# Optimization experiments

Hardware: AMD Instinct MI355X
Metric: run time of the kernel (lower is better)

## Reference

```python
import jax, jax.numpy as jnp
import numpy as np

MAX_SPAN_WIDTH = 30
NUM_WORDS = 2048
NUM_CAND = 8192
HIDDEN = 768
FEAT = 20
FFNN = 1000
SPAN_DIM = HIDDEN * 3 + FEAT  # 2324
TOP_SPAN_NUM = int(NUM_WORDS * 0.4)  # 819


def setup_inputs() -> dict:
    key = jax.random.key(0)
    ks = jax.random.split(key, 16)
    mention_doc = jax.random.normal(ks[0], (NUM_WORDS, HIDDEN), jnp.float32)
    starts = jax.random.randint(ks[1], (NUM_CAND,), 0, NUM_WORDS - MAX_SPAN_WIDTH, jnp.int32)
    widths = jax.random.randint(ks[2], (NUM_CAND,), 1, MAX_SPAN_WIDTH + 1, jnp.int32)
    ends = jnp.minimum(starts + widths - 1, NUM_WORDS - 1).astype(jnp.int32)
    s = 0.02
    lin = lambda k, i, o: jax.random.normal(k, (i, o), jnp.float32) * s
    return dict(
        mention_doc=mention_doc,
        span_width_emb=jax.random.normal(ks[3], (MAX_SPAN_WIDTH, FEAT), jnp.float32) * s,
        head_w=jax.random.normal(ks[4], (HIDDEN,), jnp.float32) * s,
        head_b=jnp.zeros((), jnp.float32),
        m_w1=lin(ks[5], SPAN_DIM, FFNN), m_b1=jnp.zeros((FFNN,), jnp.float32),
        m_w2=lin(ks[6], FFNN, FFNN), m_b2=jnp.zeros((FFNN,), jnp.float32),
        m_w3=jax.random.normal(ks[7], (FFNN,), jnp.float32) * s, m_b3=jnp.zeros((), jnp.float32),
        width_prior_emb=jax.random.normal(ks[8], (MAX_SPAN_WIDTH, FEAT), jnp.float32) * s,
        w_w1=lin(ks[9], FEAT, FFNN), w_b1=jnp.zeros((FFNN,), jnp.float32),
        w_w2=lin(ks[10], FFNN, FFNN), w_b2=jnp.zeros((FFNN,), jnp.float32),
        w_w3=jax.random.normal(ks[11], (FFNN,), jnp.float32) * s, w_b3=jnp.zeros((), jnp.float32),
        candidate_starts=starts,
        candidate_ends=ends,
        top_span_num=TOP_SPAN_NUM,
    )


def get_span_emb(mention_doc, starts, ends, span_width_emb, head_w, head_b):
    # mention_doc: [N, H]; starts/ends: [C]
    num_words = mention_doc.shape[0]
    start_emb = mention_doc[starts]              # [C, H]
    end_emb = mention_doc[ends]                  # [C, H]
    width_ids = ends - starts                    # span width - 1, in [0, MAX_SPAN_WIDTH)
    width_emb = span_width_emb[width_ids]        # [C, F]
    offs = jnp.arange(MAX_SPAN_WIDTH, dtype=starts.dtype)
    idxes = jnp.minimum(starts[:, None] + offs[None, :], num_words - 1)  # [C, W]
    emb_spans = mention_doc[idxes]               # [C, W, H]  (dominant intermediate)
    head_scores = mention_doc @ head_w + head_b  # [N]
    hs = head_scores[idxes]                      # [C, W]
    mask = offs[None, :] <= width_ids[:, None]
    hs = jnp.where(mask, hs, -jnp.inf)
    attn = jax.nn.softmax(hs, axis=1)            # masked softmax over span positions
    attended = jnp.einsum('cw,cwh->ch', attn, emb_spans)
    return jnp.concatenate([start_emb, end_emb, width_emb, attended], axis=-1)  # [C, 3H+F]


def ffnn3(x, w1, b1, w2, b2, w3, b3):
    h = jax.nn.relu(x @ w1 + b1)
    h = jax.nn.relu(h @ w2 + b2)
    return h @ w3 + b3  # [..., ] scalar score per row (Squeezer)


def extract_top_spans(span_scores, starts, ends, top_span_num, num_words):
    # Greedy crossing-interval NMS, faithful to the original sequential algorithm.
    C = span_scores.shape[0]
    order = jnp.argsort(-span_scores)
    offs = jnp.arange(MAX_SPAN_WIDTH, dtype=jnp.int32)

    def body(i, state):
        max_end, min_start, sel, count = state
        idx = order[i]
        s = starts[idx]
        e = ends[idx]
        dup = max_end[s] == e
        j_raw = s + offs
        j = jnp.minimum(j_raw, num_words - 1)
        in_span = j_raw <= e
        # crossing: an already-selected span starting at j>s ends beyond e,
        # or one ending at j<e starts before s.
        c1 = in_span & (j_raw > s) & (max_end[j] > e)
        c2 = in_span & (j_raw < e) & (min_start[j] < s)
        crossed = jnp.any(c1 | c2)
        accept = (~dup) & (~crossed) & (count < top_span_num)
        sel = jnp.where(accept, sel.at[count].set(idx.astype(jnp.int32)), sel)
        max_end = jnp.where(accept, max_end.at[s].max(e), max_end)
        min_start = jnp.where(accept, min_start.at[e].min(s), min_start)
        count = count + accept.astype(jnp.int32)
        return (max_end, min_start, sel, count)

    max_end0 = jnp.full((num_words,), -1, jnp.int32)          # 'not set' sentinel
    min_start0 = jnp.full((num_words,), num_words, jnp.int32)  # 'not set' sentinel
    sel0 = jnp.zeros((top_span_num,), jnp.int32)
    _, _, sel, count = jax.lax.fori_loop(0, C, body, (max_end0, min_start0, sel0, jnp.int32(0)))

    # sort selected spans by (start, end); pad unfilled slots with the first sorted span
    valid = jnp.arange(top_span_num) < count
    keys = jnp.where(valid, starts[sel] * num_words + ends[sel], jnp.iinfo(jnp.int32).max)
    sorted_sel = sel[jnp.argsort(keys)]
    return jnp.where(valid, sorted_sel, sorted_sel[0])


def reference(mention_doc, span_width_emb, head_w, head_b,
              m_w1, m_b1, m_w2, m_b2, m_w3, m_b3,
              width_prior_emb, w_w1, w_b1, w_w2, w_b2, w_w3, w_b3,
              candidate_starts, candidate_ends, top_span_num):
    num_words = mention_doc.shape[0]
    span_emb = get_span_emb(mention_doc, candidate_starts, candidate_ends,
                            span_width_emb, head_w, head_b)            # [C, 2324]
    mention_scores = ffnn3(span_emb, m_w1, m_b1, m_w2, m_b2, m_w3, m_b3)  # [C]
    width_scores = ffnn3(width_prior_emb, w_w1, w_b1, w_w2, w_b2, w_w3, w_b3)  # [30]
    cand_mention_scores = mention_scores + width_scores[candidate_ends - candidate_starts]
    top_idx = extract_top_spans(cand_mention_scores, candidate_starts, candidate_ends,
                                top_span_num, num_words)               # [top]
    top_starts = candidate_starts[top_idx]
    top_ends = candidate_ends[top_idx]
    top_span_emb = span_emb[top_idx]
    top_scores = cand_mention_scores[top_idx]
    return (cand_mention_scores, top_idx, top_starts, top_ends, top_span_emb, top_scores)
```

## Files before the change

### kernel.cpp

```cpp
#include <hip/hip_runtime.h>
#include <cstdio>
#include <cmath>

#define NUM_WORDS 2048
#define NUM_CAND 8192
#define HIDDEN 768
#define FEAT 20
#define FFNN_DIM 1000
#define SPAN_DIM 2324
#define TOP_NUM 819
#define MSW 30
#define KP2 1024
#define NP 1024
#define PNP 3072

#define OUT_TOPIDX   (NUM_CAND)
#define OUT_TSTART   (NUM_CAND + TOP_NUM)
#define OUT_TEND     (NUM_CAND + 2*TOP_NUM)
#define OUT_TEMB     (NUM_CAND + 3*TOP_NUM)
#define OUT_TSCORE   (NUM_CAND + 3*TOP_NUM + TOP_NUM*SPAN_DIM)

typedef short short8 __attribute__((ext_vector_type(8)));
typedef float f32x4 __attribute__((ext_vector_type(4)));
typedef unsigned short u16x4 __attribute__((ext_vector_type(4)));

__device__ __forceinline__ unsigned short bf16_rne(float x) {
    unsigned int u = __float_as_uint(x);
    unsigned int r = u + 0x7FFFu + ((u >> 16) & 1u);
    return (unsigned short)(r >> 16);
}
__device__ __forceinline__ float bf16_to_f(unsigned short h) {
    return __uint_as_float(((unsigned int)h) << 16);
}
__device__ __forceinline__ void store_split3(unsigned short* p0, unsigned short* p1,
                                             unsigned short* p2, size_t off, float v) {
    unsigned short h0 = bf16_rne(v);
    float r1 = v - bf16_to_f(h0);
    unsigned short h1 = bf16_rne(r1);
    float r2 = r1 - bf16_to_f(h1);
    p0[off] = h0;
    p1[off] = h1;
    p2[off] = bf16_rne(r2);
}

__device__ __forceinline__ void gl_lds16(const unsigned short* g, unsigned short* l) {
    __builtin_amdgcn_global_load_lds(
        (const __attribute__((address_space(1))) unsigned short*)g,
        (__attribute__((address_space(3))) unsigned short*)l, 16, 0, 0);
}

__global__ void head_kernel(const float* __restrict__ doc, const float* __restrict__ hw,
                            const float* __restrict__ hb, float* __restrict__ out) {
    int wave = threadIdx.x >> 6, lane = threadIdx.x & 63;
    int row = blockIdx.x * 4 + wave;
    if (row >= NUM_WORDS) return;
    float acc = 0.f;
    for (int h = lane; h < HIDDEN; h += 64) acc += doc[row * HIDDEN + h] * hw[h];
    for (int off = 32; off > 0; off >>= 1) acc += __shfl_down(acc, off);
    if (lane == 0) out[row] = acc + hb[0];
}

__global__ void width_kernel(const float* __restrict__ x, const float* __restrict__ w1,
                             const float* __restrict__ b1, const float* __restrict__ w2,
                             const float* __restrict__ b2, const float* __restrict__ w3,
                             const float* __restrict__ b3, float* __restrict__ out) {
    __shared__ float xs[FEAT];
    __shared__ float h1s[FFNN_DIM];
    __shared__ float red[256];
    int r = blockIdx.x, t = threadIdx.x;
    if (t < FEAT) xs[t] = x[r * FEAT + t];
    __syncthreads();
    for (int j = t; j < FFNN_DIM; j += 256) {
        float acc = b1[j];
        for (int k = 0; k < FEAT; ++k) acc += xs[k] * w1[k * FFNN_DIM + j];
        h1s[j] = fmaxf(acc, 0.f);
    }
    __syncthreads();
    float partial = 0.f;
    for (int j = t; j < FFNN_DIM; j += 256) {
        float acc = b2[j];
        for (int k = 0; k < FFNN_DIM; ++k) acc += h1s[k] * w2[k * FFNN_DIM + j];
        partial += fmaxf(acc, 0.f) * w3[j];
    }
    red[t] = partial;
    __syncthreads();
    for (int s = 128; s > 0; s >>= 1) { if (t < s) red[t] += red[t + s]; __syncthreads(); }
    if (t == 0) out[r] = red[0] + b3[0];
}

__global__ void attn_kernel(const float* __restrict__ head_s, const int* __restrict__ starts,
                            const int* __restrict__ ends, float* __restrict__ attn_g) {
    int wave = threadIdx.x >> 6, w = threadIdx.x & 63;
    int c = blockIdx.x * 4 + wave;
    if (c >= NUM_CAND) return;
    int s = starts[c], e = ends[c];
    int wid = e - s;
    float hsv = -INFINITY;
    if (w < MSW && w <= wid) hsv = head_s[s + w];
    float m = hsv;
    for (int off = 32; off > 0; off >>= 1) m = fmaxf(m, __shfl_down(m, off));
    m = __shfl(m, 0);
    float ex = (w < MSW && w <= wid) ? expf(hsv - m) : 0.f;
    float ssum = ex;
    for (int off = 32; off > 0; off >>= 1) ssum += __shfl_down(ssum, off);
    ssum = __shfl(ssum, 0);
    if (w < 32) attn_g[c * 32 + w] = (w < MSW) ? (ex / ssum) : 0.f;
}

__global__ void doc_convert(const float* __restrict__ doc, unsigned short* __restrict__ d0,
                            unsigned short* __restrict__ d1, unsigned short* __restrict__ d2) {
    int i = blockIdx.x * 256 + threadIdx.x;
    if (i < NUM_WORDS * HIDDEN) store_split3(d0, d1, d2, i, doc[i]);
}

__global__ void convert_wt(const float* __restrict__ w, int K, int N, int Kp,
                           unsigned short* __restrict__ q0, unsigned short* __restrict__ q1,
                           unsigned short* __restrict__ q2) {
    int n = blockIdx.y;
    int k = blockIdx.x * blockDim.x + threadIdx.x;
    if (k >= Kp) return;
    float v = (k < K && n < N) ? w[(size_t)k * N + n] : 0.f;
    store_split3(q0, q1, q2, (size_t)n * Kp + k, v);
}

__global__ void tw_kernel(const float* __restrict__ swe, const float* __restrict__ w1,
                          float* __restrict__ tw) {
    int wid = blockIdx.x, t = threadIdx.x;
    for (int n = t; n < NP; n += 256) {
        float acc = 0.f;
        if (n < FFNN_DIM) {
            for (int f = 0; f < FEAT; ++f)
                acc += swe[wid * FEAT + f] * w1[(size_t)(1536 + f) * FFNN_DIM + n];
        }
        tw[wid * NP + n] = acc;
    }
}

__device__ __forceinline__ void stage_tile(const unsigned short* __restrict__ src,
                                           unsigned short* lds, int base_row, int Kp, int k0,
                                           int t) {
#pragma unroll
    for (int qi = 0; qi < 2; ++qi) {
        int u = qi * 256 + t;
        int l = u & 63;
        int row = ((u >> 6) << 4) + (l >> 2);
        int cblk = (l & 3) ^ (row & 3);
        const unsigned short* g = src + (size_t)(base_row + row) * Kp + k0 + cblk * 8;
        gl_lds16(g, lds + u * 8);
    }
}

__global__ __launch_bounds__(256, 2) void gemm6p(
    const unsigned short* __restrict__ A0, const unsigned short* __restrict__ A1,
    const unsigned short* __restrict__ A2,
    const unsigned short* __restrict__ B0, const unsigned short* __restrict__ B1,
    const unsigned short* __restrict__ B2,
    float* __restrict__ C) {
    __shared__ unsigned short As0[128 * 32], As1[128 * 32], As2[128 * 32];
    __shared__ unsigned short Bs0[128 * 32], Bs1[128 * 32], Bs2[128 * 32];
    int t = threadIdx.x;
    int bid = blockIdx.x;
    int bm = (bid & 15) << 7;
    int bn = (bid >> 4) << 7;
    int lane = t & 63, wv = t >> 6;
    int wm = (wv >> 1) * 64, wn = (wv & 1) * 64;
    int lr = lane & 15, qq = lane >> 4;
    int sw = (qq ^ (lr & 3)) * 8;

    f32x4 acc[4][4] = {};

    for (int k0 = 0; k0 < HIDDEN; k0 += 32) {
        stage_tile(A0, As0, bm, HIDDEN, k0, t);
        stage_tile(A1, As1, bm, HIDDEN, k0, t);
        stage_tile(A2, As2, bm, HIDDEN, k0, t);
        stage_tile(B0, Bs0, bn, HIDDEN, k0, t);
        stage_tile(B1, Bs1, bn, HIDDEN, k0, t);
        stage_tile(B2, Bs2, bn, HIDDEN, k0, t);
        __syncthreads();
        short8 a0[4], a1[4], a2[4];
#pragma unroll
        for (int i = 0; i < 4; ++i) {
            int ra = (wm + i * 16 + lr) * 32 + sw;
            a0[i] = *(const short8*)&As0[ra];
            a1[i] = *(const short8*)&As1[ra];
            a2[i] = *(const short8*)&As2[ra];
        }
#pragma unroll
        for (int j = 0; j < 4; ++j) {
            int rb = (wn + j * 16 + lr) * 32 + sw;
            short8 b0 = *(const short8*)&Bs0[rb];
            short8 b1 = *(const short8*)&Bs1[rb];
            short8 b2 = *(const short8*)&Bs2[rb];
#pragma unroll
            for (int i = 0; i < 4; ++i) {
                acc[i][j] = __builtin_amdgcn_mfma_f32_16x16x32_bf16(a2[i], b0, acc[i][j], 0, 0, 0);
                acc[i][j] = __builtin_amdgcn_mfma_f32_16x16x32_bf16(a0[i], b2, acc[i][j], 0, 0, 0);
                acc[i][j] = __builtin_amdgcn_mfma_f32_16x16x32_bf16(a1[i], b1, acc[i][j], 0, 0, 0);
                acc[i][j] = __builtin_amdgcn_mfma_f32_16x16x32_bf16(a1[i], b0, acc[i][j], 0, 0, 0);
                acc[i][j] = __builtin_amdgcn_mfma_f32_16x16x32_bf16(a0[i], b1, acc[i][j], 0, 0, 0);
                acc[i][j] = __builtin_amdgcn_mfma_f32_16x16x32_bf16(a0[i], b0, acc[i][j], 0, 0, 0);
            }
        }
        __syncthreads();
    }
#pragma unroll
    for (int i = 0; i < 4; ++i)
#pragma unroll
        for (int j = 0; j < 4; ++j)
#pragma unroll
            for (int r = 0; r < 4; ++r) {
                int m = bm + wm + i * 16 + qq * 4 + r;
                int n = bn + wn + j * 16 + lr;
                C[(size_t)m * PNP + n] = acc[i][j][r];
            }
}

__global__ void combine_kernel(const float* __restrict__ P, const float* __restrict__ tw,
                               const float* __restrict__ attn_g, const float* __restrict__ b1,
                               const int* __restrict__ starts, const int* __restrict__ ends,
                               unsigned short* __restrict__ h0, unsigned short* __restrict__ h1,
                               unsigned short* __restrict__ h2) {
    int c = blockIdx.x, t = threadIdx.x;
    int s = starts[c], e = ends[c];
    int wid = e - s;
    __shared__ float at[MSW];
    if (t < MSW) at[t] = attn_g[c * 32 + t];
    __syncthreads();
    int n0 = t * 4;
    size_t ho = (size_t)c * NP + n0;
    if (t < 250) {
        f32x4 acc = *(const f32x4*)&P[(size_t)s * PNP + n0];
        acc += *(const f32x4*)&P[(size_t)e * PNP + 1024 + n0];
        acc += *(const f32x4*)&tw[(size_t)wid * NP + n0];
        acc += *(const f32x4*)&b1[n0];
        const float* Pa = P + (size_t)s * PNP + 2048 + n0;
        for (int w = 0; w <= wid; ++w)
            acc += at[w] * *(const f32x4*)&Pa[(size_t)w * PNP];
        u16x4 q0, q1, q2;
#pragma unroll
        for (int k = 0; k < 4; ++k) {
            float v = fmaxf(acc[k], 0.f);
            unsigned short x0 = bf16_rne(v);
            float r1 = v - bf16_to_f(x0);
            unsigned short x1 = bf16_rne(r1);
            float r2 = r1 - bf16_to_f(x1);
            q0[k] = x0; q1[k] = x1; q2[k] = bf16_rne(r2);
        }
        *(u16x4*)&h0[ho] = q0;
        *(u16x4*)&h1[ho] = q1;
        *(u16x4*)&h2[ho] = q2;
    } else {
        u16x4 z = {0, 0, 0, 0};
        *(u16x4*)&h0[ho] = z;
        *(u16x4*)&h1[ho] = z;
        *(u16x4*)&h2[ho] = z;
    }
}

__global__ __launch_bounds__(256, 2) void gemm6(
    const unsigned short* __restrict__ A0, const unsigned short* __restrict__ A1,
    const unsigned short* __restrict__ A2,
    const unsigned short* __restrict__ B0, const unsigned short* __restrict__ B1,
    const unsigned short* __restrict__ B2,
    const float* __restrict__ bias, int nreal, int Kp,
    const float* __restrict__ w3, float* __restrict__ partials) {
    __shared__ unsigned short As0[128 * 32], As1[128 * 32], As2[128 * 32];
    __shared__ unsigned short Bs0[128 * 32], Bs1[128 * 32], Bs2[128 * 32];
    int t = threadIdx.x;
    int bid = blockIdx.x;
    int sm = bid >> 6, idx = bid & 63;
    int bm = ((sm << 3) + (idx & 7)) << 7;
    int bn = (idx >> 3) << 7;
    int lane = t & 63, wv = t >> 6;
    int wm = (wv >> 1) * 64, wn = (wv & 1) * 64;
    int lr = lane & 15, qq = lane >> 4;
    int sw = (qq ^ (lr & 3)) * 8;

    f32x4 acc[4][4] = {};

    for (int k0 = 0; k0 < Kp; k0 += 32) {
        stage_tile(A0, As0, bm, Kp, k0, t);
        stage_tile(A1, As1, bm, Kp, k0, t);
        stage_tile(A2, As2, bm, Kp, k0, t);
        stage_tile(B0, Bs0, bn, Kp, k0, t);
        stage_tile(B1, Bs1, bn, Kp, k0, t);
        stage_tile(B2, Bs2, bn, Kp, k0, t);
        __syncthreads();
        short8 a0[4], a1[4], a2[4];
#pragma unroll
        for (int i = 0; i < 4; ++i) {
            int ra = (wm + i * 16 + lr) * 32 + sw;
            a0[i] = *(const short8*)&As0[ra];
            a1[i] = *(const short8*)&As1[ra];
            a2[i] = *(const short8*)&As2[ra];
        }
#pragma unroll
        for (int j = 0; j < 4; ++j) {
            int rb = (wn + j * 16 + lr) * 32 + sw;
            short8 b0 = *(const short8*)&Bs0[rb];
            short8 b1 = *(const short8*)&Bs1[rb];
            short8 b2 = *(const short8*)&Bs2[rb];
#pragma unroll
            for (int i = 0; i < 4; ++i) {
                acc[i][j] = __builtin_amdgcn_mfma_f32_16x16x32_bf16(a2[i], b0, acc[i][j], 0, 0, 0);
                acc[i][j] = __builtin_amdgcn_mfma_f32_16x16x32_bf16(a0[i], b2, acc[i][j], 0, 0, 0);
                acc[i][j] = __builtin_amdgcn_mfma_f32_16x16x32_bf16(a1[i], b1, acc[i][j], 0, 0, 0);
                acc[i][j] = __builtin_amdgcn_mfma_f32_16x16x32_bf16(a1[i], b0, acc[i][j], 0, 0, 0);
                acc[i][j] = __builtin_amdgcn_mfma_f32_16x16x32_bf16(a0[i], b1, acc[i][j], 0, 0, 0);
                acc[i][j] = __builtin_amdgcn_mfma_f32_16x16x32_bf16(a0[i], b0, acc[i][j], 0, 0, 0);
            }
        }
        __syncthreads();
    }

    int pid = ((bn >> 7) << 1) | (wn >> 6);
#pragma unroll
    for (int i = 0; i < 4; ++i)
#pragma unroll
        for (int r = 0; r < 4; ++r) {
            float p = 0.f;
#pragma unroll
            for (int j = 0; j < 4; ++j) {
                int n = bn + wn + j * 16 + lr;
                float v = acc[i][j][r] + (n < nreal ? bias[n] : 0.f);
                v = fmaxf(v, 0.f);
                p += v * (n < nreal ? w3[n] : 0.f);
            }
            p += __shfl_xor(p, 1);
            p += __shfl_xor(p, 2);
            p += __shfl_xor(p, 4);
            p += __shfl_xor(p, 8);
            if (lr == 0) {
                int m = bm + wm + i * 16 + qq * 4 + r;
                partials[(size_t)m * 16 + pid] = p;
            }
        }
}

__global__ void score_final(const float* __restrict__ partials, const float* __restrict__ b3,
                            const float* __restrict__ width_s, const int* __restrict__ starts,
                            const int* __restrict__ ends, float* __restrict__ out) {
    int c = blockIdx.x * 256 + threadIdx.x;
    if (c >= NUM_CAND) return;
    float s = b3[0] + width_s[ends[c] - starts[c]];
#pragma unroll
    for (int p = 0; p < 16; ++p) s += partials[(size_t)c * 16 + p];
    out[c] = s;
}

__global__ __launch_bounds__(256) void rank_kernel(const float* __restrict__ scores,
                                                   const int* __restrict__ starts,
                                                   const int* __restrict__ ends,
                                                   unsigned short* __restrict__ ord_g,
                                                   unsigned int* __restrict__ se_g) {
    __shared__ unsigned long long kk[NUM_CAND];
    int t = threadIdx.x;
    for (int i = t; i < NUM_CAND; i += 256) {
        unsigned int b = __float_as_uint(scores[i]);
        unsigned int u = b ^ ((b & 0x80000000u) ? 0xFFFFFFFFu : 0x80000000u);
        unsigned int hi = ~u;
        kk[i] = ((unsigned long long)hi << 32) | (unsigned int)i;
    }
    __syncthreads();
    int c = blockIdx.x * 32 + (t >> 3);
    int seg = (t & 7) * 1024;
    unsigned long long mykey = kk[c];
    int cnt = 0;
    for (int i = seg; i < seg + 1024; ++i) cnt += (kk[i] < mykey) ? 1 : 0;
    cnt += __shfl_xor(cnt, 1);
    cnt += __shfl_xor(cnt, 2);
    cnt += __shfl_xor(cnt, 4);
    if ((t & 7) == 0) {
        int idx = (int)(mykey & 0xFFFFFFFFull);
        int rank = cnt;
        ord_g[rank] = (unsigned short)idx;
        se_g[rank] = ((unsigned int)starts[idx] << 16) | (unsigned int)ends[idx];
    }
}

__global__ __launch_bounds__(512)
__attribute__((amdgpu_waves_per_eu(1, 2)))
void select_nms(const unsigned int* __restrict__ se_g,
                unsigned short* __restrict__ sel_g,
                int* __restrict__ count_g) {
    __shared__ unsigned int se_arr[NUM_CAND];
    __shared__ unsigned int st[2 * NUM_WORDS];
    __shared__ unsigned int lst[512];
    __shared__ int pos[9];
    __shared__ int count_sh;
    int t = threadIdx.x;
    int wv = t >> 6, lane = t & 63;

    for (int i = t; i < NUM_CAND; i += 512) se_arr[i] = se_g[i];
    for (int i = t; i < 2 * NUM_WORDS; i += 512)
        st[i] = (i & 1) ? (unsigned int)NUM_WORDS : 0u;
    if (t == 0) count_sh = 0;
    __syncthreads();

    const unsigned long long* stp = (const unsigned long long*)st;
    for (int r = 0; r < NUM_CAND / 512; ++r) {
        int ib = r * 512 + wv * 64;
        unsigned int sev = se_arr[ib + lane];
        int s = (int)(sev >> 16), e = (int)(sev & 0xFFFFu);
        const unsigned long long* bp = stp + s;
        unsigned long long v[MSW];
#pragma unroll
        for (int w = 0; w < MSW; ++w) v[w] = bp[w];
        int me = (int)(unsigned int)v[0] - 1;
        bool crossed = (s < e) && ((int)(unsigned int)(v[0] >> 32) < s);
#pragma unroll
        for (int w = 1; w < MSW; ++w) {
            int j = s + w;
            bool in = (j <= e);
            int mej = (int)(unsigned int)v[w] - 1;
            int msj = (int)(unsigned int)(v[w] >> 32);
            crossed = crossed || (in && ((mej > e) || ((j < e) && (msj < s))));
        }
        bool spec = !crossed && (me != e);
        if (t == 0) pos[0] = 0;
        __syncthreads();

        for (int p = 0; p < 8; ++p) {
            if (p > 0 && wv >= p) {
                int lo = pos[p - 1], hi = pos[p];
                for (int k = lo; k < hi; ++k) {
                    unsigned int sef = lst[k];
                    int sf = (int)(sef >> 16), ef = (int)(sef & 0xFFFFu);
                    if (s == sf) me = max(me, ef);
                    crossed = crossed || ((s < sf) && (sf <= e) && (ef > e))
                                      || ((sf < s) && (s <= ef) && (ef < e));
                }
                spec = !crossed && (me != e);
            }
            if (wv == p) {
                int cbefore = count_sh;
                int lbase = pos[p];
                if (cbefore < TOP_NUM) {
                    int count = cbefore;
                    unsigned long long window = ~0ull;
                    unsigned int pend = 0u;
                    int rk = 0, lcnt = 0;
                    while (true) {
                        unsigned long long b = __ballot(spec) & window;
                        if (b == 0ull) break;
                        int f = __ffsll((unsigned long long)b) - 1;
                        unsigned int sef = __builtin_amdgcn_readlane(sev, (unsigned int)f);
                        int sf = (int)(sef >> 16), ef = (int)(sef & 0xFFFFu);
                        bool mine = (lane == lcnt);
                        pend = mine ? sef : pend;
                        rk = mine ? (ib + f) : rk;
                        lcnt++;
                        count++;
                        if (count >= TOP_NUM) break;
                        window &= (f >= 63) ? 0ull : (~0ull << (f + 1));
                        if (lane > f) {
                            if (s == sf) me = max(me, ef);
                            crossed = crossed || ((s < sf) && (sf <= e) && (ef > e))
                                              || ((sf < s) && (s <= ef) && (ef < e));
                            spec = !crossed && (me != e);
                        }
                    }
                    if (lane < lcnt) {
                        int sf = (int)(pend >> 16), ef = (int)(pend & 0xFFFFu);
                        sel_g[cbefore + lane] = (unsigned short)rk;
                        lst[lbase + lane] = pend;
                        atomicMax(&st[2 * sf], (unsigned int)(ef + 1));
                        atomicMin(&st[2 * ef + 1], (unsigned int)sf);
                    }
                    if (lane == 0) {
                        count_sh = count;
                        pos[p + 1] = lbase + lcnt;
                    }
                } else {
                    if (lane == 0) pos[p + 1] = lbase;
                }
            }
            __syncthreads();
        }
        if (count_sh >= TOP_NUM) break;
    }
    if (t == 0) *count_g = count_sh;
}

__global__ __launch_bounds__(256) void select_post(const float* __restrict__ scores,
                                                   const int* __restrict__ starts,
                                                   const int* __restrict__ ends,
                                                   const unsigned short* __restrict__ ord_g,
                                                   const unsigned short* __restrict__ sel_g,
                                                   const int* __restrict__ count_g,
                                                   float* out, int* top_idx_ws) {
    __shared__ unsigned long long fkeys[1024];
    int t = threadIdx.x;
    int count = *count_g;
    for (int i = t; i < 1024; i += 256) {
        unsigned long long k = 0xFFFFFFFFFFFFFFFFull;
        if (i < count) {
            int idx = (int)ord_g[sel_g[i]];
            unsigned int key32 = (unsigned int)(starts[idx] * NUM_WORDS + ends[idx]);
            k = ((unsigned long long)key32 << 32) | (unsigned int)idx;
        }
        fkeys[i] = k;
    }
    __syncthreads();
    for (int size = 2; size <= 1024; size <<= 1) {
        for (int stride = size >> 1; stride > 0; stride >>= 1) {
            for (int i = t; i < 1024; i += 256) {
                int ixj = i ^ stride;
                if (ixj > i) {
                    bool up = ((i & size) == 0);
                    unsigned long long a = fkeys[i], b = fkeys[ixj];
                    if ((a > b) == up) { fkeys[i] = b; fkeys[ixj] = a; }
                }
            }
            __syncthreads();
        }
    }
    for (int i = t; i < TOP_NUM; i += 256) {
        int fi = (i < count) ? (int)(fkeys[i] & 0xFFFFFFFFull)
                             : (int)(fkeys[0] & 0xFFFFFFFFull);
        out[OUT_TOPIDX + i] = (float)fi;
        out[OUT_TSTART + i] = (float)starts[fi];
        out[OUT_TEND + i] = (float)ends[fi];
        out[OUT_TSCORE + i] = scores[fi];
        top_idx_ws[i] = fi;
    }
}

__global__ void gather_emb(const float* __restrict__ doc, const float* __restrict__ swe,
                           const float* __restrict__ attn_g, const int* __restrict__ starts,
                           const int* __restrict__ ends, const int* __restrict__ top_idx_ws,
                           float* __restrict__ out) {
    int r = blockIdx.x, t = threadIdx.x;
    int idx = top_idx_ws[r];
    int s = starts[idx], e = ends[idx];
    int wid = e - s;
    __shared__ float at[MSW];
    if (t < MSW) at[t] = attn_g[(size_t)idx * 32 + t];
    __syncthreads();
    float* dst = out + OUT_TEMB + (size_t)r * SPAN_DIM;
    if (t < 192) {
        int h4 = t * 4;
        f32x4 vs = *(const f32x4*)&doc[(size_t)s * HIDDEN + h4];
        f32x4 ve = *(const f32x4*)&doc[(size_t)e * HIDDEN + h4];
        f32x4 acc = {0.f, 0.f, 0.f, 0.f};
        for (int w = 0; w <= wid; ++w)
            acc += at[w] * *(const f32x4*)&doc[(size_t)(s + w) * HIDDEN + h4];
#pragma unroll
        for (int k = 0; k < 4; ++k) {
            dst[h4 + k] = vs[k];
            dst[HIDDEN + h4 + k] = ve[k];
            dst[2 * HIDDEN + FEAT + h4 + k] = acc[k];
        }
    }
    if (t < FEAT) dst[2 * HIDDEN + t] = swe[wid * FEAT + t];
}

extern "C" void kernel_launch(void* const* d_in, const int* in_sizes, int n_in,
                              void* d_out, int out_size, void* d_ws, size_t ws_size,
                              hipStream_t stream) {
    const float* mention_doc = (const float*)d_in[0];
    const float* span_width_emb = (const float*)d_in[1];
    const float* head_w = (const float*)d_in[2];
    const float* head_b = (const float*)d_in[3];
    const float* m_w1 = (const float*)d_in[4];
    const float* m_b1 = (const float*)d_in[5];
    const float* m_w2 = (const float*)d_in[6];
    const float* m_b2 = (const float*)d_in[7];
    const float* m_w3 = (const float*)d_in[8];
    const float* m_b3 = (const float*)d_in[9];
    const float* width_prior_emb = (const float*)d_in[10];
    const float* w_w1 = (const float*)d_in[11];
    const float* w_b1 = (const float*)d_in[12];
    const float* w_w2 = (const float*)d_in[13];
    const float* w_b2 = (const float*)d_in[14];
    const float* w_w3 = (const float*)d_in[15];
    const float* w_b3 = (const float*)d_in[16];
    const int* cand_starts = (const int*)d_in[17];
    const int* cand_ends = (const int*)d_in[18];

    char* w = (char*)d_ws;
    const size_t szH = (size_t)NUM_CAND * NP * 2;
    const size_t szW2 = (size_t)NP * KP2 * 2;
    const size_t szWc = (size_t)PNP * HIDDEN * 2;
    const size_t szD = (size_t)NUM_WORDS * HIDDEN * 2;
    char* p = w;
    unsigned short* h0 = (unsigned short*)p; p += szH;
    unsigned short* h1 = (unsigned short*)p; p += szH;
    unsigned short* h2 = (unsigned short*)p; p += szH;
    unsigned short* w2t0 = (unsigned short*)p; p += szW2;
    unsigned short* w2t1 = (unsigned short*)p; p += szW2;
    unsigned short* w2t2 = (unsigned short*)p; p += szW2;
    unsigned short* Wc0 = (unsigned short*)p; p += szWc;
    unsigned short* Wc1 = (unsigned short*)p; p += szWc;
    unsigned short* Wc2 = (unsigned short*)p; p += szWc;
    unsigned short* d0 = (unsigned short*)p; p += szD;
    unsigned short* d1 = (unsigned short*)p; p += szD;
    unsigned short* d2 = (unsigned short*)p; p += szD;
    float* P = (float*)p; p += (size_t)NUM_WORDS * PNP * 4;
    float* tw = (float*)p; p += (size_t)MSW * NP * 4;
    float* attn_g = (float*)p; p += (size_t)NUM_CAND * 32 * 4;
    float* partials = (float*)p; p += (size_t)NUM_CAND * 16 * 4;
    unsigned short* ord_g = (unsigned short*)p; p += (size_t)NUM_CAND * 2;
    unsigned int* se_g = (unsigned int*)p; p += (size_t)NUM_CAND * 4;
    unsigned short* sel_g = (unsigned short*)p; p += 2048;
    int* count_g = (int*)p; p += 128;
    float* head_s = (float*)p; p += NUM_WORDS * 4;
    float* width_s = (float*)p; p += 128;
    int* top_idx_ws = (int*)p; p += 4096;

    size_t need = (size_t)(p - w);
    if (ws_size < need) {
        fprintf(stderr, "kernel_launch: ws too small (%zu < %zu)\n", ws_size, need);
    }

    float* out = (float*)d_out;

    head_kernel<<<NUM_WORDS / 4, 256, 0, stream>>>(mention_doc, head_w, head_b, head_s);
    width_kernel<<<MSW, 256, 0, stream>>>(width_prior_emb, w_w1, w_b1, w_w2, w_b2, w_w3, w_b3,
                                          width_s);
    attn_kernel<<<NUM_CAND / 4, 256, 0, stream>>>(head_s, cand_starts, cand_ends, attn_g);
    doc_convert<<<(NUM_WORDS * HIDDEN + 255) / 256, 256, 0, stream>>>(mention_doc, d0, d1, d2);
    convert_wt<<<dim3(3, 1024), 256, 0, stream>>>(m_w1, HIDDEN, FFNN_DIM, HIDDEN,
                                                  Wc0, Wc1, Wc2);
    convert_wt<<<dim3(3, 1024), 256, 0, stream>>>(m_w1 + (size_t)HIDDEN * FFNN_DIM, HIDDEN,
                                                  FFNN_DIM, HIDDEN,
                                                  Wc0 + (size_t)1024 * HIDDEN,
                                                  Wc1 + (size_t)1024 * HIDDEN,
                                                  Wc2 + (size_t)1024 * HIDDEN);
    convert_wt<<<dim3(3, 1024), 256, 0, stream>>>(m_w1 + (size_t)1556 * FFNN_DIM, HIDDEN,
                                                  FFNN_DIM, HIDDEN,
                                                  Wc0 + (size_t)2048 * HIDDEN,
                                                  Wc1 + (size_t)2048 * HIDDEN,
                                                  Wc2 + (size_t)2048 * HIDDEN);
    convert_wt<<<dim3(4, 1024), 256, 0, stream>>>(m_w2, FFNN_DIM, FFNN_DIM, KP2,
                                                  w2t0, w2t1, w2t2);
    tw_kernel<<<MSW, 256, 0, stream>>>(span_width_emb, m_w1, tw);
    gemm6p<<<16 * 24, 256, 0, stream>>>(d0, d1, d2, Wc0, Wc1, Wc2, P);
    combine_kernel<<<NUM_CAND, 256, 0, stream>>>(P, tw, attn_g, m_b1, cand_starts, cand_ends,
                                                 h0, h1, h2);
    gemm6<<<512, 256, 0, stream>>>(h0, h1, h2, w2t0, w2t1, w2t2, m_b2, FFNN_DIM, KP2,
                                   m_w3, partials);
    score_final<<<NUM_CAND / 256, 256, 0, stream>>>(partials, m_b3, width_s, cand_starts,
                                                    cand_ends, out);
    rank_kernel<<<NUM_CAND / 32, 256, 0, stream>>>(out, cand_starts, cand_ends, ord_g, se_g);
    select_nms<<<1, 512, 0, stream>>>(se_g, sel_g, count_g);
    select_post<<<1, 256, 0, stream>>>(out, cand_starts, cand_ends, ord_g, sel_g, count_g,
                                       out, top_idx_ws);
    gather_emb<<<TOP_NUM, 256, 0, stream>>>(mention_doc, span_width_emb, attn_g, cand_starts,
                                            cand_ends, top_idx_ws, out);
}
```

Measured before the change: 889.6 us.

## Run sequential span NMS in a single wavefront without block barriers

Rewrites the greedy crossing-span selection kernel to use one 64-lane wavefront that walks candidate chunks in order, in place of eight waves that speculatively precompute and then reconcile through shared lists and a barrier per wave. This removes per-round __syncthreads and the cross-wave fix-up loop. The cost is that per-chunk crossing checks are no longer computed in parallel by other waves. It also splits the crossing-test OR chain into two accumulators and vectorises the initial shared-memory load.

```diff
diff --git a/kernel.cpp b/kernel.cpp
--- a/kernel.cpp
+++ b/kernel.cpp
@@ -378,28 +378,27 @@
     }
 }
 
-__global__ __launch_bounds__(512)
-__attribute__((amdgpu_waves_per_eu(1, 2)))
+__global__ __launch_bounds__(64, 1)
 void select_nms(const unsigned int* __restrict__ se_g,
                 unsigned short* __restrict__ sel_g,
                 int* __restrict__ count_g) {
     __shared__ unsigned int se_arr[NUM_CAND];
     __shared__ unsigned int st[2 * NUM_WORDS];
-    __shared__ unsigned int lst[512];
-    __shared__ int pos[9];
-    __shared__ int count_sh;
-    int t = threadIdx.x;
-    int wv = t >> 6, lane = t & 63;
-
-    for (int i = t; i < NUM_CAND; i += 512) se_arr[i] = se_g[i];
-    for (int i = t; i < 2 * NUM_WORDS; i += 512)
+    int lane = threadIdx.x;
+
+    {
+        const uint4* src4 = (const uint4*)se_g;
+        uint4* dst4 = (uint4*)se_arr;
+        for (int i = lane; i < NUM_CAND / 4; i += 64) dst4[i] = src4[i];
+    }
+    for (int i = lane; i < 2 * NUM_WORDS; i += 64)
         st[i] = (i & 1) ? (unsigned int)NUM_WORDS : 0u;
-    if (t == 0) count_sh = 0;
     __syncthreads();
 
     const unsigned long long* stp = (const unsigned long long*)st;
-    for (int r = 0; r < NUM_CAND / 512; ++r) {
-        int ib = r * 512 + wv * 64;
+    int count = 0;
+    for (int c = 0; c < NUM_CAND / 64; ++c) {
+        int ib = c * 64;
         unsigned int sev = se_arr[ib + lane];
         int s = (int)(sev >> 16), e = (int)(sev & 0xFFFFu);
         const unsigned long long* bp = stp + s;
@@ -407,79 +406,54 @@
 #pragma unroll
         for (int w = 0; w < MSW; ++w) v[w] = bp[w];
         int me = (int)(unsigned int)v[0] - 1;
-        bool crossed = (s < e) && ((int)(unsigned int)(v[0] >> 32) < s);
+        bool crossedA = (s < e) && ((int)(unsigned int)(v[0] >> 32) < s);
+        bool crossedB = false;
 #pragma unroll
         for (int w = 1; w < MSW; ++w) {
             int j = s + w;
             bool in = (j <= e);
             int mej = (int)(unsigned int)v[w] - 1;
             int msj = (int)(unsigned int)(v[w] >> 32);
-            crossed = crossed || (in && ((mej > e) || ((j < e) && (msj < s))));
-        }
+            bool hit = in && ((mej > e) || ((j < e) && (msj < s)));
+            if (w & 1) crossedA = crossedA || hit;
+            else       crossedB = crossedB || hit;
+        }
+        bool crossed = crossedA || crossedB;
         bool spec = !crossed && (me != e);
-        if (t == 0) pos[0] = 0;
-        __syncthreads();
-
-        for (int p = 0; p < 8; ++p) {
-            if (p > 0 && wv >= p) {
-                int lo = pos[p - 1], hi = pos[p];
-                for (int k = lo; k < hi; ++k) {
-                    unsigned int sef = lst[k];
-                    int sf = (int)(sef >> 16), ef = (int)(sef & 0xFFFFu);
-                    if (s == sf) me = max(me, ef);
-                    crossed = crossed || ((s < sf) && (sf <= e) && (ef > e))
-                                      || ((sf < s) && (s <= ef) && (ef < e));
-                }
+
+        int cbefore = count;
+        unsigned long long window = ~0ull;
+        unsigned int pend = 0u;
+        int rk = 0, lcnt = 0;
+        while (true) {
+            unsigned long long b = __ballot(spec) & window;
+            if (b == 0ull) break;
+            int f = __ffsll((unsigned long long)b) - 1;
+            unsigned int sef = __builtin_amdgcn_readlane(sev, (unsigned int)f);
+            int sf = (int)(sef >> 16), ef = (int)(sef & 0xFFFFu);
+            bool mine = (lane == lcnt);
+            pend = mine ? sef : pend;
+            rk = mine ? (ib + f) : rk;
+            lcnt++;
+            count++;
+            if (count >= TOP_NUM) break;
+            window &= (f >= 63) ? 0ull : (~0ull << (f + 1));
+            if (lane > f) {
+                if (s == sf) me = max(me, ef);
+                crossed = crossed || ((s < sf) && (sf <= e) && (ef > e))
+                                  || ((sf < s) && (s <= ef) && (ef < e));
                 spec = !crossed && (me != e);
             }
-            if (wv == p) {
-                int cbefore = count_sh;
-                int lbase = pos[p];
-                if (cbefore < TOP_NUM) {
-                    int count = cbefore;
-                    unsigned long long window = ~0ull;
-                    unsigned int pend = 0u;
-                    int rk = 0, lcnt = 0;
-                    while (true) {
-                        unsigned long long b = __ballot(spec) & window;
-                        if (b == 0ull) break;
-                        int f = __ffsll((unsigned long long)b) - 1;
-                        unsigned int sef = __builtin_amdgcn_readlane(sev, (unsigned int)f);
-                        int sf = (int)(sef >> 16), ef = (int)(sef & 0xFFFFu);
-                        bool mine = (lane == lcnt);
-                        pend = mine ? sef : pend;
-                        rk = mine ? (ib + f) : rk;
-                        lcnt++;
-                        count++;
-                        if (count >= TOP_NUM) break;
-                        window &= (f >= 63) ? 0ull : (~0ull << (f + 1));
-                        if (lane > f) {
-                            if (s == sf) me = max(me, ef);
-                            crossed = crossed || ((s < sf) && (sf <= e) && (ef > e))
-                                              || ((sf < s) && (s <= ef) && (ef < e));
-                            spec = !crossed && (me != e);
-                        }
-                    }
-                    if (lane < lcnt) {
-                        int sf = (int)(pend >> 16), ef = (int)(pend & 0xFFFFu);
-                        sel_g[cbefore + lane] = (unsigned short)rk;
-                        lst[lbase + lane] = pend;
-                        atomicMax(&st[2 * sf], (unsigned int)(ef + 1));
-                        atomicMin(&st[2 * ef + 1], (unsigned int)sf);
-                    }
-                    if (lane == 0) {
-                        count_sh = count;
-                        pos[p + 1] = lbase + lcnt;
-                    }
-                } else {
-                    if (lane == 0) pos[p + 1] = lbase;
-                }
-            }
-            __syncthreads();
-        }
-        if (count_sh >= TOP_NUM) break;
-    }
-    if (t == 0) *count_g = count_sh;
+        }
+        if (lane < lcnt) {
+            int sf = (int)(pend >> 16), ef = (int)(pend & 0xFFFFu);
+            sel_g[cbefore + lane] = (unsigned short)rk;
+            atomicMax(&st[2 * sf], (unsigned int)(ef + 1));
+            atomicMin(&st[2 * ef + 1], (unsigned int)sf);
+        }
+        if (count >= TOP_NUM) break;
+    }
+    if (lane == 0) *count_g = count;
 }
 
 __global__ __launch_bounds__(256) void select_post(const float* __restrict__ scores,
@@ -643,7 +617,7 @@
     score_final<<<NUM_CAND / 256, 256, 0, stream>>>(partials, m_b3, width_s, cand_starts,
                                                     cand_ends, out);
     rank_kernel<<<NUM_CAND / 32, 256, 0, stream>>>(out, cand_starts, cand_ends, ord_g, se_g);
-    select_nms<<<1, 512, 0, stream>>>(se_g, sel_g, count_g);
+    select_nms<<<1, 64, 0, stream>>>(se_g, sel_g, count_g);
     select_post<<<1, 256, 0, stream>>>(out, cand_starts, cand_ends, ord_g, sel_g, count_g,
                                        out, top_idx_ws);
     gather_emb<<<TOP_NUM, 256, 0, stream>>>(mention_doc, span_width_emb, attn_g, cand_starts,
```

Result: faster. 869.7 us (-2.2%).
